# Kernel optimization log

Measured on AMD Instinct MI355X. Metric: run time of the kernel, lower is better.

The kernel has to match this reference:

```python
import jax, jax.numpy as jnp
import numpy as np

B, T, C = 4, 4096, 256

def setup_inputs() -> dict:
    key = jax.random.key(0)
    kx, km, kk, kq, kv = jax.random.split(key, 5)
    x = jax.random.normal(kx, (B, T, C), dtype=jnp.float32)
    mask = jax.random.randint(km, (B, T), 0, 2, dtype=jnp.int32)
    s = C ** -0.5
    Wk = jax.random.normal(kk, (C, C), dtype=jnp.float32) * s
    Wq = jax.random.normal(kq, (C, C), dtype=jnp.float32) * s
    Wv = jax.random.normal(kv, (C, C), dtype=jnp.float32) * s
    return {"x": x, "mask": mask, "Wk": Wk, "Wq": Wq, "Wv": Wv}

def reference(x, mask, Wk, Wq, Wv):
    # nn.Linear: y = x @ W.T  (W is [out, in])
    k = jnp.einsum('btc,dc->btd', x, Wk)   # [B,T,C]
    q = jnp.einsum('btc,dc->btd', x, Wq)   # [B,T,C]
    v = jnp.einsum('btc,dc->btd', x, Wv)   # [B,T,C]
    scale = k.shape[-1] ** -0.5
    weights = jnp.einsum('bqc,bkc->bqk', q, k) * scale  # [B,T,T]
    # torch quirk: mask.float().masked_fill(mask==0, -inf) adds +1.0 where mask!=0
    mask_f = jnp.where(mask == 0, -jnp.inf, mask.astype(weights.dtype))  # [B,T]
    masked = weights + mask_f[:, None, :]   # broadcast over query dim == repeat(1,T,1)
    attn = jax.nn.softmax(masked, axis=-1)
    out = jnp.einsum('bqk,bkc->bqc', attn, v)  # [B,T,C]
    return out
```

## Files before the change

### kernel.cpp

```cpp
#include <hip/hip_runtime.h>


typedef __attribute__((ext_vector_type(8)))  _Float16 f16x8;
typedef __attribute__((ext_vector_type(4)))  _Float16 f16x4;
typedef __attribute__((ext_vector_type(4)))  float    f32x4;
typedef __attribute__((ext_vector_type(16))) float    f32x16;

constexpr int Bb = 4;
constexpr int Tt = 4096;
constexpr int Cc = 256;
constexpr int BT = Bb * Tt;

#define MFMA16(a, b, c) __builtin_amdgcn_mfma_f32_16x16x32_f16((a), (b), (c), 0, 0, 0)
#define MFMA32(a, b, c) __builtin_amdgcn_mfma_f32_32x32x16_f16((a), (b), (c), 0, 0, 0)

__global__ __launch_bounds__(256) void qkv_proj(
    const float* __restrict__ x,
    const float* __restrict__ Wq, const float* __restrict__ Wk,
    const float* __restrict__ Wv,
    _Float16* __restrict__ qo, _Float16* __restrict__ ko,
    _Float16* __restrict__ vto)
{
    extern __shared__ _Float16 sm[];
    _Float16* xs = sm;
    _Float16* wsm = sm + 128 * 264;

    const int tid = threadIdx.x;
    const int m0  = blockIdx.x * 128;
    const int ny  = blockIdx.y;
    const int mat = ny >> 1;
    const int d0  = (ny & 1) * 128;
    const float* W = (mat == 0) ? Wq : (mat == 1 ? Wk : Wv);

#pragma unroll
    for (int i = 0; i < 32; ++i) {
        int flat = i * 256 + tid;
        int r = flat >> 6, c4 = (flat & 63) << 2;
        float4 v = *reinterpret_cast<const float4*>(x + (size_t)(m0 + r) * Cc + c4);
        f16x4 h = { (_Float16)v.x, (_Float16)v.y, (_Float16)v.z, (_Float16)v.w };
        *reinterpret_cast<f16x4*>(xs + r * 264 + c4) = h;
    }
#pragma unroll
    for (int i = 0; i < 32; ++i) {
        int flat = i * 256 + tid;
        int r = flat >> 6, c4 = (flat & 63) << 2;
        float4 v = *reinterpret_cast<const float4*>(W + (size_t)(d0 + r) * Cc + c4);
        f16x4 h = { (_Float16)v.x, (_Float16)v.y, (_Float16)v.z, (_Float16)v.w };
        *reinterpret_cast<f16x4*>(wsm + r * 264 + c4) = h;
    }
    __syncthreads();

    const int w = tid >> 6, lane = tid & 63;
    const int lr = lane & 15, lg = lane >> 4;

    f32x4 acc[2][8] = {};

#pragma unroll
    for (int kc = 0; kc < 8; ++kc) {
        const int c0 = kc * 32 + lg * 8;
        f16x8 xf[2], wf[8];
#pragma unroll
        for (int mb = 0; mb < 2; ++mb)
            xf[mb] = *reinterpret_cast<const f16x8*>(xs + (w * 32 + mb * 16 + lr) * 264 + c0);
#pragma unroll
        for (int db = 0; db < 8; ++db)
            wf[db] = *reinterpret_cast<const f16x8*>(wsm + (db * 16 + lr) * 264 + c0);
        if (mat != 2) {
#pragma unroll
            for (int mb = 0; mb < 2; ++mb)
#pragma unroll
                for (int db = 0; db < 8; ++db)
                    acc[mb][db] = MFMA16(wf[db], xf[mb], acc[mb][db]);
        } else {
#pragma unroll
            for (int mb = 0; mb < 2; ++mb)
#pragma unroll
                for (int db = 0; db < 8; ++db)
                    acc[mb][db] = MFMA16(xf[mb], wf[db], acc[mb][db]);
        }
    }

    if (mat != 2) {
        const float sc = (mat == 0) ? 0.0625f : 1.0f;
        const int jj  = (lg & 1) * 4;
#pragma unroll
        for (int mb = 0; mb < 2; ++mb)
#pragma unroll
            for (int db = 0; db < 8; ++db) {
                int m  = m0 + w * 32 + mb * 16 + lr;
                int c  = d0 + db * 16 + lg * 4;
                int kc = c >> 5;
                int ch = (c >> 3) & 3;
                f32x4 a = acc[mb][db];
                f16x4 h = { (_Float16)(a.x * sc), (_Float16)(a.y * sc),
                            (_Float16)(a.z * sc), (_Float16)(a.w * sc) };
                if (mat == 0) {
                    size_t off = (size_t)(m >> 5) * 8192 + (((m >> 4) & 1) * 8 + kc) * 512
                               + ch * 128 + (m & 15) * 8 + jj;
                    *reinterpret_cast<f16x4*>(qo + off) = h;
                } else {
                    size_t off = (size_t)(m >> 4) * 4096 + kc * 512
                               + ch * 128 + (m & 15) * 8 + jj;
                    *reinterpret_cast<f16x4*>(ko + off) = h;
                }
            }
    } else {
        const int jj = (lg & 1) * 4;
        const int kh = (lg >> 1) & 1;
#pragma unroll
        for (int mb = 0; mb < 2; ++mb)
#pragma unroll
            for (int db = 0; db < 8; ++db) {
                int d = d0 + db * 16 + lr;
                int m = m0 + w * 32 + mb * 16 + lg * 4;
                f32x4 a = acc[mb][db];
                f16x4 h = { (_Float16)a.x, (_Float16)a.y, (_Float16)a.z, (_Float16)a.w };
                size_t off = (size_t)(m >> 4) * 4096 + (d >> 5) * 512
                           + kh * 256 + (d & 31) * 8 + jj;
                *reinterpret_cast<f16x4*>(vto + off) = h;
            }
    }
}

__global__ __launch_bounds__(256, 1) void attn_kernel(
    const _Float16* __restrict__ qb, const _Float16* __restrict__ kb,
    const _Float16* __restrict__ vtb, const int* __restrict__ mask,
    float* __restrict__ outp)
{
    extern __shared__ char smraw[];
    float* mex  = (float*)(smraw + 6144);
    float* lex  = (float*)(smraw + 6656);
    float* oexf = (float*)(smraw + 8192);

    const int tid = threadIdx.x, w = tid >> 6, lane = tid & 63;
    const int qw = w >> 1, g = w & 1;
    const int l15 = lane & 15, l4 = lane >> 4;
    const int l31 = lane & 31, l5 = lane >> 5;

    const int bid = blockIdx.x;
    const int b   = (bid & 7) >> 1;
    const int qt  = ((bid >> 3) << 1) | (bid & 1);
    const int q0  = qt * 64;
    const size_t base = (size_t)b * Tt * Cc;
    const int* maskb = mask + (size_t)b * Tt;
    const _Float16* kTb = kb + base;
    const _Float16* vTb = vtb + base;

    f16x8 qf[2][8];
    {
        const _Float16* qTb = qb + (size_t)(b * 128 + qt * 2 + qw) * 8192;
#pragma unroll
        for (int qh = 0; qh < 2; ++qh)
#pragma unroll
            for (int kc = 0; kc < 8; ++kc)
                qf[qh][kc] = *reinterpret_cast<const f16x8*>(
                    qTb + (qh * 8 + kc) * 512 + l4 * 128 + l15 * 8);
    }

    _Float16* pw = (_Float16*)smraw + w * 768;

    f32x16 o[8] = {};
    float m0r = -60.f, m1r = -60.f, l0r = 0.f, l1r = 0.f;

    auto LOADT = [&](f16x8 (&kr)[8], f16x8 (&vr)[8], int4& mc, int tile) {
        const _Float16* kp = kTb + (size_t)tile * 4096 + l4 * 128 + l15 * 8;
#pragma unroll
        for (int kc = 0; kc < 8; ++kc)
            kr[kc] = *reinterpret_cast<const f16x8*>(kp + kc * 512);
        const _Float16* vp = vTb + (size_t)tile * 4096 + l5 * 256 + l31 * 8;
#pragma unroll
        for (int dt = 0; dt < 8; ++dt)
            vr[dt] = *reinterpret_cast<const f16x8*>(vp + dt * 512);
        mc = *reinterpret_cast<const int4*>(maskb + tile * 16 + l4 * 4);
    };

    auto COMPUTE = [&](f16x8 (&kr)[8], f16x8 (&vr)[8], int4 mc) {
        f32x4 s40 = { 0.f, 0.f, 0.f, 0.f }, s41 = { 0.f, 0.f, 0.f, 0.f };
#pragma unroll
        for (int kc = 0; kc < 8; ++kc) {
            s40 = MFMA16(kr[kc], qf[0][kc], s40);
            s41 = MFMA16(kr[kc], qf[1][kc], s41);
        }
        if (mc.x == 0) { s40[0] = -1e30f; s41[0] = -1e30f; }
        if (mc.y == 0) { s40[1] = -1e30f; s41[1] = -1e30f; }
        if (mc.z == 0) { s40[2] = -1e30f; s41[2] = -1e30f; }
        if (mc.w == 0) { s40[3] = -1e30f; s41[3] = -1e30f; }

        float t0 = fmaxf(fmaxf(s40[0], s40[1]), fmaxf(s40[2], s40[3]));
        float t1 = fmaxf(fmaxf(s41[0], s41[1]), fmaxf(s41[2], s41[3]));
        t0 = fmaxf(t0, __shfl_xor(t0, 16, 64)); t0 = fmaxf(t0, __shfl_xor(t0, 32, 64));
        t1 = fmaxf(t1, __shfl_xor(t1, 16, 64)); t1 = fmaxf(t1, __shfl_xor(t1, 32, 64));

        if (__any(t0 > m0r + 8.f || t1 > m1r + 8.f)) {
            float mn0 = fmaxf(m0r, t0), mn1 = fmaxf(m1r, t1);
            float c0 = __expf(m0r - mn0), c1 = __expf(m1r - mn1);
            m0r = mn0; m1r = mn1; l0r *= c0; l1r *= c1;
            float cs = (lane & 16) ? c1 : c0;
#pragma unroll
            for (int dt = 0; dt < 8; ++dt) o[dt] *= cs;
        }

        float rs0 = 0.f, rs1 = 0.f;
#pragma unroll
        for (int r = 0; r < 4; ++r) {
            float p0 = __expf(s40[r] - m0r); s40[r] = p0; rs0 += p0;
            float p1 = __expf(s41[r] - m1r); s41[r] = p1; rs1 += p1;
        }
        rs0 += __shfl_xor(rs0, 16, 64); rs0 += __shfl_xor(rs0, 32, 64);
        rs1 += __shfl_xor(rs1, 16, 64); rs1 += __shfl_xor(rs1, 32, 64);
        l0r += rs0; l1r += rs1;

        {
            f16x4 h0 = { (_Float16)s40[0], (_Float16)s40[1], (_Float16)s40[2], (_Float16)s40[3] };
            f16x4 h1 = { (_Float16)s41[0], (_Float16)s41[1], (_Float16)s41[2], (_Float16)s41[3] };
            *reinterpret_cast<f16x4*>(pw + l15 * 24 + l4 * 4)        = h0;
            *reinterpret_cast<f16x4*>(pw + (16 + l15) * 24 + l4 * 4) = h1;
        }
        f16x8 pf = *reinterpret_cast<const f16x8*>(pw + l31 * 24 + l5 * 8);

#pragma unroll
        for (int dt = 0; dt < 8; ++dt)
            o[dt] = MFMA32(vr[dt], pf, o[dt]);
    };

    f16x8 kA[8], vA[8], kB[8], vB[8];
    int4 mA_, mB_;
    const int ktb = g * 128;
    LOADT(kA, vA, mA_, ktb);
#pragma unroll 1
    for (int t2 = 0; t2 < 64; ++t2) {
        LOADT(kB, vB, mB_, ktb + 2 * t2 + 1);
        COMPUTE(kA, vA, mA_);
        LOADT(kA, vA, mA_, (2 * t2 + 2 < 128) ? (ktb + 2 * t2 + 2) : ktb);
        COMPUTE(kB, vB, mB_);
    }

    __syncthreads();
    if (l4 == 0) {
        mex[w * 32 + l15]      = m0r;  mex[w * 32 + 16 + l15] = m1r;
        lex[w * 32 + l15]      = l0r;  lex[w * 32 + 16 + l15] = l1r;
    }
    __syncthreads();

    {
        float mq  = (lane & 16) ? m1r : m0r;
        float mA2 = mex[(qw * 2 + 0) * 32 + l31];
        float mB2 = mex[(qw * 2 + 1) * 32 + l31];
        float mst = fmaxf(mA2, mB2);
        float osc = __expf(mq - mst);
        float* oq = oexf + qw * (32 * 258);
        if (g == 1) {
#pragma unroll
            for (int dt = 0; dt < 8; ++dt)
#pragma unroll
                for (int r = 0; r < 16; ++r) {
                    int d = dt * 32 + (r & 3) + 8 * (r >> 2) + 4 * l5;
                    oq[l31 * 258 + d] = o[dt][r] * osc;
                }
        }
        __syncthreads();
        if (g == 0) {
#pragma unroll
            for (int dt = 0; dt < 8; ++dt)
#pragma unroll
                for (int r = 0; r < 16; ++r) {
                    int d = dt * 32 + (r & 3) + 8 * (r >> 2) + 4 * l5;
                    oq[l31 * 258 + d] += o[dt][r] * osc;
                }
        }
        __syncthreads();
    }

    {
        const int q = tid >> 2, ds0 = (tid & 3) * 64;
        const int qws = q >> 5, ql = q & 31;
        float mA2 = mex[(qws * 2 + 0) * 32 + ql];
        float mB2 = mex[(qws * 2 + 1) * 32 + ql];
        float ms  = fmaxf(mA2, mB2);
        float lt  = lex[(qws * 2 + 0) * 32 + ql] * __expf(mA2 - ms)
                  + lex[(qws * 2 + 1) * 32 + ql] * __expf(mB2 - ms);
        float inv = 1.f / lt;
        const float* src = oexf + qws * (32 * 258) + ql * 258 + ds0;
        float* dst = outp + base + (size_t)(q0 + q) * Cc + ds0;
#pragma unroll
        for (int i = 0; i < 16; ++i) {
            f32x4 a = *reinterpret_cast<const f32x4*>(src + 4 * i);
            a[0] *= inv; a[1] *= inv; a[2] *= inv; a[3] *= inv;
            *reinterpret_cast<f32x4*>(dst + 4 * i) = a;
        }
    }
}

extern "C" void kernel_launch(void* const* d_in, const int* in_sizes, int n_in,
                              void* d_out, int out_size, void* d_ws, size_t ws_size,
                              hipStream_t stream)
{
    (void)in_sizes; (void)n_in; (void)out_size; (void)ws_size;
    const float* x   = (const float*)d_in[0];
    const int*  mask = (const int*)d_in[1];
    const float* Wk  = (const float*)d_in[2];
    const float* Wq  = (const float*)d_in[3];
    const float* Wv  = (const float*)d_in[4];
    float* out = (float*)d_out;

    _Float16* q  = (_Float16*)d_ws;
    _Float16* k  = q + (size_t)BT * Cc;
    _Float16* vt = k + (size_t)BT * Cc;

    dim3 gA(128, 6), blkA(256);
    size_t ldsA = (size_t)(128 + 128) * 264 * sizeof(_Float16);
    qkv_proj<<<gA, blkA, ldsA, stream>>>(x, Wq, Wk, Wv, q, k, vt);

    dim3 gB(256), blkB(256);
    size_t ldsB = 74240;
    attn_kernel<<<gB, blkB, ldsB, stream>>>(q, k, vt, mask, out);
}
```

Before: 128.5 us.

## Split attention work across head-dim halves, double blocks, use exp2 softmax

The attention kernel now handles 32 queries per block instead of 64. Each pair of waves splits the 256-wide value dimension into two halves, which halves the output accumulators and value registers. The launch goes to 512 blocks with launch bounds of 2 and a smaller LDS footprint. Value loads move inside the compute step rather than being double-buffered. The Q scale now folds in log2(e) so softmax can use exp2f, the rescale threshold is loosened to match, and the row-sum shuffle reduction is deferred until after the loop. These changes aim for higher occupancy and less per-iteration shuffle work. The costs are duplicated QK^T computation across the two d-halves and less latency hiding for the V loads.

```diff
diff --git a/kernel.cpp b/kernel.cpp
--- a/kernel.cpp
+++ b/kernel.cpp
@@ -81,7 +81,7 @@
     }
 
     if (mat != 2) {
-        const float sc = (mat == 0) ? 0.0625f : 1.0f;
+        const float sc = (mat == 0) ? 0.0625f * 1.44269504f : 1.0f;
         const int jj  = (lg & 1) * 4;
 #pragma unroll
         for (int mb = 0; mb < 2; ++mb)
@@ -122,25 +122,25 @@
     }
 }
 
-__global__ __launch_bounds__(256, 1) void attn_kernel(
+__global__ __launch_bounds__(256, 2) void attn_kernel(
     const _Float16* __restrict__ qb, const _Float16* __restrict__ kb,
     const _Float16* __restrict__ vtb, const int* __restrict__ mask,
     float* __restrict__ outp)
 {
     extern __shared__ char smraw[];
     float* mex  = (float*)(smraw + 6144);
-    float* lex  = (float*)(smraw + 6656);
-    float* oexf = (float*)(smraw + 8192);
+    float* lex  = (float*)(smraw + 6400);
+    float* oexf = (float*)(smraw + 6656);
 
     const int tid = threadIdx.x, w = tid >> 6, lane = tid & 63;
-    const int qw = w >> 1, g = w & 1;
+    const int dh = w & 1, g = w >> 1;
     const int l15 = lane & 15, l4 = lane >> 4;
     const int l31 = lane & 31, l5 = lane >> 5;
 
     const int bid = blockIdx.x;
     const int b   = (bid & 7) >> 1;
     const int qt  = ((bid >> 3) << 1) | (bid & 1);
-    const int q0  = qt * 64;
+    const int q0  = qt * 32;
     const size_t base = (size_t)b * Tt * Cc;
     const int* maskb = mask + (size_t)b * Tt;
     const _Float16* kTb = kb + base;
@@ -148,7 +148,7 @@
 
     f16x8 qf[2][8];
     {
-        const _Float16* qTb = qb + (size_t)(b * 128 + qt * 2 + qw) * 8192;
+        const _Float16* qTb = qb + (size_t)(b * 128 + qt) * 8192;
 #pragma unroll
         for (int qh = 0; qh < 2; ++qh)
 #pragma unroll
@@ -159,22 +159,27 @@
 
     _Float16* pw = (_Float16*)smraw + w * 768;
 
-    f32x16 o[8] = {};
+    f32x16 o[4] = {};
     float m0r = -60.f, m1r = -60.f, l0r = 0.f, l1r = 0.f;
 
-    auto LOADT = [&](f16x8 (&kr)[8], f16x8 (&vr)[8], int4& mc, int tile) {
+    auto LOADK = [&](f16x8 (&kr)[8], int4& mc, int tile) {
         const _Float16* kp = kTb + (size_t)tile * 4096 + l4 * 128 + l15 * 8;
 #pragma unroll
         for (int kc = 0; kc < 8; ++kc)
             kr[kc] = *reinterpret_cast<const f16x8*>(kp + kc * 512);
-        const _Float16* vp = vTb + (size_t)tile * 4096 + l5 * 256 + l31 * 8;
-#pragma unroll
-        for (int dt = 0; dt < 8; ++dt)
-            vr[dt] = *reinterpret_cast<const f16x8*>(vp + dt * 512);
         mc = *reinterpret_cast<const int4*>(maskb + tile * 16 + l4 * 4);
     };
 
-    auto COMPUTE = [&](f16x8 (&kr)[8], f16x8 (&vr)[8], int4 mc) {
+    f16x8 vr[4];
+    auto COMPUTE = [&](f16x8 (&kr)[8], int4 mc, int tile) {
+        {
+            const _Float16* vp = vTb + (size_t)tile * 4096 + dh * 2048
+                               + l5 * 256 + l31 * 8;
+#pragma unroll
+            for (int dt = 0; dt < 4; ++dt)
+                vr[dt] = *reinterpret_cast<const f16x8*>(vp + dt * 512);
+        }
+
         f32x4 s40 = { 0.f, 0.f, 0.f, 0.f }, s41 = { 0.f, 0.f, 0.f, 0.f };
 #pragma unroll
         for (int kc = 0; kc < 8; ++kc) {
@@ -186,29 +191,25 @@
         if (mc.z == 0) { s40[2] = -1e30f; s41[2] = -1e30f; }
         if (mc.w == 0) { s40[3] = -1e30f; s41[3] = -1e30f; }
 
-        float t0 = fmaxf(fmaxf(s40[0], s40[1]), fmaxf(s40[2], s40[3]));
-        float t1 = fmaxf(fmaxf(s41[0], s41[1]), fmaxf(s41[2], s41[3]));
-        t0 = fmaxf(t0, __shfl_xor(t0, 16, 64)); t0 = fmaxf(t0, __shfl_xor(t0, 32, 64));
-        t1 = fmaxf(t1, __shfl_xor(t1, 16, 64)); t1 = fmaxf(t1, __shfl_xor(t1, 32, 64));
-
-        if (__any(t0 > m0r + 8.f || t1 > m1r + 8.f)) {
+        float t0l = fmaxf(fmaxf(s40[0], s40[1]), fmaxf(s40[2], s40[3]));
+        float t1l = fmaxf(fmaxf(s41[0], s41[1]), fmaxf(s41[2], s41[3]));
+        if (__any(t0l > m0r + 11.54f || t1l > m1r + 11.54f)) {
+            float t0 = t0l, t1 = t1l;
+            t0 = fmaxf(t0, __shfl_xor(t0, 16, 64)); t0 = fmaxf(t0, __shfl_xor(t0, 32, 64));
+            t1 = fmaxf(t1, __shfl_xor(t1, 16, 64)); t1 = fmaxf(t1, __shfl_xor(t1, 32, 64));
             float mn0 = fmaxf(m0r, t0), mn1 = fmaxf(m1r, t1);
-            float c0 = __expf(m0r - mn0), c1 = __expf(m1r - mn1);
+            float c0 = exp2f(m0r - mn0), c1 = exp2f(m1r - mn1);
             m0r = mn0; m1r = mn1; l0r *= c0; l1r *= c1;
             float cs = (lane & 16) ? c1 : c0;
 #pragma unroll
-            for (int dt = 0; dt < 8; ++dt) o[dt] *= cs;
-        }
-
-        float rs0 = 0.f, rs1 = 0.f;
+            for (int dt = 0; dt < 4; ++dt) o[dt] *= cs;
+        }
+
 #pragma unroll
         for (int r = 0; r < 4; ++r) {
-            float p0 = __expf(s40[r] - m0r); s40[r] = p0; rs0 += p0;
-            float p1 = __expf(s41[r] - m1r); s41[r] = p1; rs1 += p1;
-        }
-        rs0 += __shfl_xor(rs0, 16, 64); rs0 += __shfl_xor(rs0, 32, 64);
-        rs1 += __shfl_xor(rs1, 16, 64); rs1 += __shfl_xor(rs1, 32, 64);
-        l0r += rs0; l1r += rs1;
+            float p0 = exp2f(s40[r] - m0r); s40[r] = p0; l0r += p0;
+            float p1 = exp2f(s41[r] - m1r); s41[r] = p1; l1r += p1;
+        }
 
         {
             f16x4 h0 = { (_Float16)s40[0], (_Float16)s40[1], (_Float16)s40[2], (_Float16)s40[3] };
@@ -219,71 +220,69 @@
         f16x8 pf = *reinterpret_cast<const f16x8*>(pw + l31 * 24 + l5 * 8);
 
 #pragma unroll
-        for (int dt = 0; dt < 8; ++dt)
+        for (int dt = 0; dt < 4; ++dt)
             o[dt] = MFMA32(vr[dt], pf, o[dt]);
     };
 
-    f16x8 kA[8], vA[8], kB[8], vB[8];
+    f16x8 kA[8], kB[8];
     int4 mA_, mB_;
     const int ktb = g * 128;
-    LOADT(kA, vA, mA_, ktb);
+    LOADK(kA, mA_, ktb);
 #pragma unroll 1
     for (int t2 = 0; t2 < 64; ++t2) {
-        LOADT(kB, vB, mB_, ktb + 2 * t2 + 1);
-        COMPUTE(kA, vA, mA_);
-        LOADT(kA, vA, mA_, (2 * t2 + 2 < 128) ? (ktb + 2 * t2 + 2) : ktb);
-        COMPUTE(kB, vB, mB_);
-    }
-
+        LOADK(kB, mB_, ktb + 2 * t2 + 1);
+        COMPUTE(kA, mA_, ktb + 2 * t2);
+        LOADK(kA, mA_, (2 * t2 + 2 < 128) ? (ktb + 2 * t2 + 2) : ktb);
+        COMPUTE(kB, mB_, ktb + 2 * t2 + 1);
+    }
+
+    float L0 = l0r; L0 += __shfl_xor(L0, 16, 64); L0 += __shfl_xor(L0, 32, 64);
+    float L1 = l1r; L1 += __shfl_xor(L1, 16, 64); L1 += __shfl_xor(L1, 32, 64);
+
+    if (dh == 0 && l4 == 0) {
+        mex[g * 32 + l15]      = m0r;  mex[g * 32 + 16 + l15] = m1r;
+        lex[g * 32 + l15]      = L0;   lex[g * 32 + 16 + l15] = L1;
+    }
     __syncthreads();
-    if (l4 == 0) {
-        mex[w * 32 + l15]      = m0r;  mex[w * 32 + 16 + l15] = m1r;
-        lex[w * 32 + l15]      = l0r;  lex[w * 32 + 16 + l15] = l1r;
-    }
-    __syncthreads();
 
     {
+        float mst = fmaxf(mex[l31], mex[32 + l31]);
         float mq  = (lane & 16) ? m1r : m0r;
-        float mA2 = mex[(qw * 2 + 0) * 32 + l31];
-        float mB2 = mex[(qw * 2 + 1) * 32 + l31];
-        float mst = fmaxf(mA2, mB2);
-        float osc = __expf(mq - mst);
-        float* oq = oexf + qw * (32 * 258);
+        float osc = exp2f(mq - mst);
+        float* oq = oexf + dh * 4224;
         if (g == 1) {
 #pragma unroll
-            for (int dt = 0; dt < 8; ++dt)
+            for (int dt = 0; dt < 4; ++dt)
 #pragma unroll
                 for (int r = 0; r < 16; ++r) {
-                    int d = dt * 32 + (r & 3) + 8 * (r >> 2) + 4 * l5;
-                    oq[l31 * 258 + d] = o[dt][r] * osc;
+                    int dloc = dt * 32 + (r & 3) + 8 * (r >> 2) + 4 * l5;
+                    oq[l31 * 132 + dloc] = o[dt][r] * osc;
                 }
         }
         __syncthreads();
         if (g == 0) {
 #pragma unroll
-            for (int dt = 0; dt < 8; ++dt)
+            for (int dt = 0; dt < 4; ++dt)
 #pragma unroll
                 for (int r = 0; r < 16; ++r) {
-                    int d = dt * 32 + (r & 3) + 8 * (r >> 2) + 4 * l5;
-                    oq[l31 * 258 + d] += o[dt][r] * osc;
+                    int dloc = dt * 32 + (r & 3) + 8 * (r >> 2) + 4 * l5;
+                    oq[l31 * 132 + dloc] += o[dt][r] * osc;
                 }
         }
         __syncthreads();
     }
 
     {
-        const int q = tid >> 2, ds0 = (tid & 3) * 64;
-        const int qws = q >> 5, ql = q & 31;
-        float mA2 = mex[(qws * 2 + 0) * 32 + ql];
-        float mB2 = mex[(qws * 2 + 1) * 32 + ql];
+        const int q = tid >> 3, seg = tid & 7;
+        const int ds0 = seg * 32, dhr = seg >> 2, dl0 = (seg & 3) * 32;
+        float mA2 = mex[q], mB2 = mex[32 + q];
         float ms  = fmaxf(mA2, mB2);
-        float lt  = lex[(qws * 2 + 0) * 32 + ql] * __expf(mA2 - ms)
-                  + lex[(qws * 2 + 1) * 32 + ql] * __expf(mB2 - ms);
+        float lt  = lex[q] * exp2f(mA2 - ms) + lex[32 + q] * exp2f(mB2 - ms);
         float inv = 1.f / lt;
-        const float* src = oexf + qws * (32 * 258) + ql * 258 + ds0;
+        const float* src = oexf + dhr * 4224 + q * 132 + dl0;
         float* dst = outp + base + (size_t)(q0 + q) * Cc + ds0;
 #pragma unroll
-        for (int i = 0; i < 16; ++i) {
+        for (int i = 0; i < 8; ++i) {
             f32x4 a = *reinterpret_cast<const f32x4*>(src + 4 * i);
             a[0] *= inv; a[1] *= inv; a[2] *= inv; a[3] *= inv;
             *reinterpret_cast<f32x4*>(dst + 4 * i) = a;
@@ -311,7 +310,7 @@
     size_t ldsA = (size_t)(128 + 128) * 264 * sizeof(_Float16);
     qkv_proj<<<gA, blkA, ldsA, stream>>>(x, Wq, Wk, Wv, q, k, vt);
 
-    dim3 gB(256), blkB(256);
-    size_t ldsB = 74240;
+    dim3 gB(512), blkB(256);
+    size_t ldsB = 40448;
     attn_kernel<<<gB, blkB, ldsB, stream>>>(q, k, vt, mask, out);
 }
```

Result: slower. 157.2 us (+22.4%).

## Feed P to PV MFMA from registers using 16x16x16 and exp2 softmax

Applied to the files above, without the earlier changes.

Reworks the PV product to use 16x16x16 MFMAs whose A operand is the score accumulator layout directly, which removes the LDS round trip for the probability tile. The V layout from the projection kernel changes to match, and the query scale folds in log2(e) so the softmax can use exp2. Row sums are kept per lane and reduced only once at the end. The max reduction across lanes now runs only when a rescale is triggered. The QK accumulation is split into two chains to increase MFMA ILP. In exchange it issues twice as many smaller MFMAs for PV and adds shuffles to broadcast the rescale factors.

```diff
diff --git a/kernel.cpp b/kernel.cpp
--- a/kernel.cpp
+++ b/kernel.cpp
@@ -4,15 +4,14 @@
 typedef __attribute__((ext_vector_type(8)))  _Float16 f16x8;
 typedef __attribute__((ext_vector_type(4)))  _Float16 f16x4;
 typedef __attribute__((ext_vector_type(4)))  float    f32x4;
-typedef __attribute__((ext_vector_type(16))) float    f32x16;
 
 constexpr int Bb = 4;
 constexpr int Tt = 4096;
 constexpr int Cc = 256;
 constexpr int BT = Bb * Tt;
 
-#define MFMA16(a, b, c) __builtin_amdgcn_mfma_f32_16x16x32_f16((a), (b), (c), 0, 0, 0)
-#define MFMA32(a, b, c) __builtin_amdgcn_mfma_f32_32x32x16_f16((a), (b), (c), 0, 0, 0)
+#define MFMA16(a, b, c)   __builtin_amdgcn_mfma_f32_16x16x32_f16((a), (b), (c), 0, 0, 0)
+#define MFMA1616(a, b, c) __builtin_amdgcn_mfma_f32_16x16x16f16((a), (b), (c), 0, 0, 0)
 
 __global__ __launch_bounds__(256) void qkv_proj(
     const float* __restrict__ x,
@@ -81,7 +80,7 @@
     }
 
     if (mat != 2) {
-        const float sc = (mat == 0) ? 0.0625f : 1.0f;
+        const float sc = (mat == 0) ? 0.0625f * 1.44269504f : 1.0f;
         const int jj  = (lg & 1) * 4;
 #pragma unroll
         for (int mb = 0; mb < 2; ++mb)
@@ -105,8 +104,6 @@
                 }
             }
     } else {
-        const int jj = (lg & 1) * 4;
-        const int kh = (lg >> 1) & 1;
 #pragma unroll
         for (int mb = 0; mb < 2; ++mb)
 #pragma unroll
@@ -115,8 +112,8 @@
                 int m = m0 + w * 32 + mb * 16 + lg * 4;
                 f32x4 a = acc[mb][db];
                 f16x4 h = { (_Float16)a.x, (_Float16)a.y, (_Float16)a.z, (_Float16)a.w };
-                size_t off = (size_t)(m >> 4) * 4096 + (d >> 5) * 512
-                           + kh * 256 + (d & 31) * 8 + jj;
+                size_t off = (size_t)(m >> 4) * 4096 + (size_t)(d >> 4) * 256
+                           + lg * 64 + (d & 15) * 4;
                 *reinterpret_cast<f16x4*>(vto + off) = h;
             }
     }
@@ -128,14 +125,13 @@
     float* __restrict__ outp)
 {
     extern __shared__ char smraw[];
-    float* mex  = (float*)(smraw + 6144);
-    float* lex  = (float*)(smraw + 6656);
-    float* oexf = (float*)(smraw + 8192);
+    float* mex  = (float*)(smraw);
+    float* lex  = (float*)(smraw + 512);
+    float* oexf = (float*)(smraw + 1024);
 
     const int tid = threadIdx.x, w = tid >> 6, lane = tid & 63;
     const int qw = w >> 1, g = w & 1;
     const int l15 = lane & 15, l4 = lane >> 4;
-    const int l31 = lane & 31, l5 = lane >> 5;
 
     const int bid = blockIdx.x;
     const int b   = (bid & 7) >> 1;
@@ -157,73 +153,78 @@
                     qTb + (qh * 8 + kc) * 512 + l4 * 128 + l15 * 8);
     }
 
-    _Float16* pw = (_Float16*)smraw + w * 768;
-
-    f32x16 o[8] = {};
+    f32x4 o[2][16] = {};
     float m0r = -60.f, m1r = -60.f, l0r = 0.f, l1r = 0.f;
 
-    auto LOADT = [&](f16x8 (&kr)[8], f16x8 (&vr)[8], int4& mc, int tile) {
+    auto LOADT = [&](f16x8 (&kr)[8], f16x4 (&vr)[16], int4& mc, int tile) {
         const _Float16* kp = kTb + (size_t)tile * 4096 + l4 * 128 + l15 * 8;
 #pragma unroll
         for (int kc = 0; kc < 8; ++kc)
             kr[kc] = *reinterpret_cast<const f16x8*>(kp + kc * 512);
-        const _Float16* vp = vTb + (size_t)tile * 4096 + l5 * 256 + l31 * 8;
-#pragma unroll
-        for (int dt = 0; dt < 8; ++dt)
-            vr[dt] = *reinterpret_cast<const f16x8*>(vp + dt * 512);
+        const _Float16* vp = vTb + (size_t)tile * 4096 + l4 * 64 + l15 * 4;
+#pragma unroll
+        for (int dt = 0; dt < 16; ++dt)
+            vr[dt] = *reinterpret_cast<const f16x4*>(vp + dt * 256);
         mc = *reinterpret_cast<const int4*>(maskb + tile * 16 + l4 * 4);
     };
 
-    auto COMPUTE = [&](f16x8 (&kr)[8], f16x8 (&vr)[8], int4 mc) {
-        f32x4 s40 = { 0.f, 0.f, 0.f, 0.f }, s41 = { 0.f, 0.f, 0.f, 0.f };
-#pragma unroll
-        for (int kc = 0; kc < 8; ++kc) {
-            s40 = MFMA16(kr[kc], qf[0][kc], s40);
-            s41 = MFMA16(kr[kc], qf[1][kc], s41);
-        }
+    auto COMPUTE = [&](f16x8 (&kr)[8], f16x4 (&vr)[16], int4 mc) {
+        f32x4 a0 = { 0.f, 0.f, 0.f, 0.f }, b0 = { 0.f, 0.f, 0.f, 0.f };
+        f32x4 a1 = { 0.f, 0.f, 0.f, 0.f }, b1 = { 0.f, 0.f, 0.f, 0.f };
+#pragma unroll
+        for (int kc = 0; kc < 4; ++kc) {
+            a0 = MFMA16(kr[kc], qf[0][kc], a0);
+            a1 = MFMA16(kr[kc], qf[1][kc], a1);
+        }
+#pragma unroll
+        for (int kc = 4; kc < 8; ++kc) {
+            b0 = MFMA16(kr[kc], qf[0][kc], b0);
+            b1 = MFMA16(kr[kc], qf[1][kc], b1);
+        }
+        f32x4 s40 = a0 + b0, s41 = a1 + b1;
+
         if (mc.x == 0) { s40[0] = -1e30f; s41[0] = -1e30f; }
         if (mc.y == 0) { s40[1] = -1e30f; s41[1] = -1e30f; }
         if (mc.z == 0) { s40[2] = -1e30f; s41[2] = -1e30f; }
         if (mc.w == 0) { s40[3] = -1e30f; s41[3] = -1e30f; }
 
-        float t0 = fmaxf(fmaxf(s40[0], s40[1]), fmaxf(s40[2], s40[3]));
-        float t1 = fmaxf(fmaxf(s41[0], s41[1]), fmaxf(s41[2], s41[3]));
-        t0 = fmaxf(t0, __shfl_xor(t0, 16, 64)); t0 = fmaxf(t0, __shfl_xor(t0, 32, 64));
-        t1 = fmaxf(t1, __shfl_xor(t1, 16, 64)); t1 = fmaxf(t1, __shfl_xor(t1, 32, 64));
-
-        if (__any(t0 > m0r + 8.f || t1 > m1r + 8.f)) {
+        float t0l = fmaxf(fmaxf(s40[0], s40[1]), fmaxf(s40[2], s40[3]));
+        float t1l = fmaxf(fmaxf(s41[0], s41[1]), fmaxf(s41[2], s41[3]));
+        if (__any(t0l > m0r + 11.54f || t1l > m1r + 11.54f)) {
+            float t0 = t0l, t1 = t1l;
+            t0 = fmaxf(t0, __shfl_xor(t0, 16, 64)); t0 = fmaxf(t0, __shfl_xor(t0, 32, 64));
+            t1 = fmaxf(t1, __shfl_xor(t1, 16, 64)); t1 = fmaxf(t1, __shfl_xor(t1, 32, 64));
             float mn0 = fmaxf(m0r, t0), mn1 = fmaxf(m1r, t1);
-            float c0 = __expf(m0r - mn0), c1 = __expf(m1r - mn1);
+            float c0 = exp2f(m0r - mn0), c1 = exp2f(m1r - mn1);
             m0r = mn0; m1r = mn1; l0r *= c0; l1r *= c1;
-            float cs = (lane & 16) ? c1 : c0;
-#pragma unroll
-            for (int dt = 0; dt < 8; ++dt) o[dt] *= cs;
-        }
-
-        float rs0 = 0.f, rs1 = 0.f;
+            f32x4 cv0, cv1;
+#pragma unroll
+            for (int r = 0; r < 4; ++r) {
+                cv0[r] = __shfl(c0, l4 * 4 + r, 64);
+                cv1[r] = __shfl(c1, l4 * 4 + r, 64);
+            }
+#pragma unroll
+            for (int dt = 0; dt < 16; ++dt) { o[0][dt] *= cv0; o[1][dt] *= cv1; }
+        }
+
 #pragma unroll
         for (int r = 0; r < 4; ++r) {
-            float p0 = __expf(s40[r] - m0r); s40[r] = p0; rs0 += p0;
-            float p1 = __expf(s41[r] - m1r); s41[r] = p1; rs1 += p1;
-        }
-        rs0 += __shfl_xor(rs0, 16, 64); rs0 += __shfl_xor(rs0, 32, 64);
-        rs1 += __shfl_xor(rs1, 16, 64); rs1 += __shfl_xor(rs1, 32, 64);
-        l0r += rs0; l1r += rs1;
-
-        {
-            f16x4 h0 = { (_Float16)s40[0], (_Float16)s40[1], (_Float16)s40[2], (_Float16)s40[3] };
-            f16x4 h1 = { (_Float16)s41[0], (_Float16)s41[1], (_Float16)s41[2], (_Float16)s41[3] };
-            *reinterpret_cast<f16x4*>(pw + l15 * 24 + l4 * 4)        = h0;
-            *reinterpret_cast<f16x4*>(pw + (16 + l15) * 24 + l4 * 4) = h1;
-        }
-        f16x8 pf = *reinterpret_cast<const f16x8*>(pw + l31 * 24 + l5 * 8);
-
-#pragma unroll
-        for (int dt = 0; dt < 8; ++dt)
-            o[dt] = MFMA32(vr[dt], pf, o[dt]);
+            float p0 = exp2f(s40[r] - m0r); s40[r] = p0; l0r += p0;
+            float p1 = exp2f(s41[r] - m1r); s41[r] = p1; l1r += p1;
+        }
+
+        f16x4 pa0 = { (_Float16)s40[0], (_Float16)s40[1], (_Float16)s40[2], (_Float16)s40[3] };
+        f16x4 pa1 = { (_Float16)s41[0], (_Float16)s41[1], (_Float16)s41[2], (_Float16)s41[3] };
+
+#pragma unroll
+        for (int dt = 0; dt < 16; ++dt) {
+            o[0][dt] = MFMA1616(pa0, vr[dt], o[0][dt]);
+            o[1][dt] = MFMA1616(pa1, vr[dt], o[1][dt]);
+        }
     };
 
-    f16x8 kA[8], vA[8], kB[8], vB[8];
+    f16x8 kA[8], kB[8];
+    f16x4 vA[16], vB[16];
     int4 mA_, mB_;
     const int ktb = g * 128;
     LOADT(kA, vA, mA_, ktb);
@@ -235,38 +236,48 @@
         COMPUTE(kB, vB, mB_);
     }
 
+    float L0 = l0r; L0 += __shfl_xor(L0, 16, 64); L0 += __shfl_xor(L0, 32, 64);
+    float L1 = l1r; L1 += __shfl_xor(L1, 16, 64); L1 += __shfl_xor(L1, 32, 64);
+
     __syncthreads();
-    if (l4 == 0) {
-        mex[w * 32 + l15]      = m0r;  mex[w * 32 + 16 + l15] = m1r;
-        lex[w * 32 + l15]      = l0r;  lex[w * 32 + 16 + l15] = l1r;
+    if (lane < 16) {
+        mex[w * 32 + lane]      = m0r;  mex[w * 32 + 16 + lane] = m1r;
+        lex[w * 32 + lane]      = L0;   lex[w * 32 + 16 + lane] = L1;
     }
     __syncthreads();
 
     {
-        float mq  = (lane & 16) ? m1r : m0r;
-        float mA2 = mex[(qw * 2 + 0) * 32 + l31];
-        float mB2 = mex[(qw * 2 + 1) * 32 + l31];
-        float mst = fmaxf(mA2, mB2);
-        float osc = __expf(mq - mst);
         float* oq = oexf + qw * (32 * 258);
+        f32x4 osc[2];
+#pragma unroll
+        for (int qh = 0; qh < 2; ++qh)
+#pragma unroll
+            for (int r = 0; r < 4; ++r) {
+                int qq = qh * 16 + l4 * 4 + r;
+                float mO = mex[(qw * 2 + g) * 32 + qq];
+                float mX = mex[(qw * 2 + (1 - g)) * 32 + qq];
+                osc[qh][r] = exp2f(mO - fmaxf(mO, mX));
+            }
         if (g == 1) {
 #pragma unroll
-            for (int dt = 0; dt < 8; ++dt)
-#pragma unroll
-                for (int r = 0; r < 16; ++r) {
-                    int d = dt * 32 + (r & 3) + 8 * (r >> 2) + 4 * l5;
-                    oq[l31 * 258 + d] = o[dt][r] * osc;
-                }
+            for (int qh = 0; qh < 2; ++qh)
+#pragma unroll
+                for (int dt = 0; dt < 16; ++dt)
+#pragma unroll
+                    for (int r = 0; r < 4; ++r)
+                        oq[(qh * 16 + l4 * 4 + r) * 258 + dt * 16 + l15]
+                            = o[qh][dt][r] * osc[qh][r];
         }
         __syncthreads();
         if (g == 0) {
 #pragma unroll
-            for (int dt = 0; dt < 8; ++dt)
-#pragma unroll
-                for (int r = 0; r < 16; ++r) {
-                    int d = dt * 32 + (r & 3) + 8 * (r >> 2) + 4 * l5;
-                    oq[l31 * 258 + d] += o[dt][r] * osc;
-                }
+            for (int qh = 0; qh < 2; ++qh)
+#pragma unroll
+                for (int dt = 0; dt < 16; ++dt)
+#pragma unroll
+                    for (int r = 0; r < 4; ++r)
+                        oq[(qh * 16 + l4 * 4 + r) * 258 + dt * 16 + l15]
+                            += o[qh][dt][r] * osc[qh][r];
         }
         __syncthreads();
     }
@@ -277,8 +288,8 @@
         float mA2 = mex[(qws * 2 + 0) * 32 + ql];
         float mB2 = mex[(qws * 2 + 1) * 32 + ql];
         float ms  = fmaxf(mA2, mB2);
-        float lt  = lex[(qws * 2 + 0) * 32 + ql] * __expf(mA2 - ms)
-                  + lex[(qws * 2 + 1) * 32 + ql] * __expf(mB2 - ms);
+        float lt  = lex[(qws * 2 + 0) * 32 + ql] * exp2f(mA2 - ms)
+                  + lex[(qws * 2 + 1) * 32 + ql] * exp2f(mB2 - ms);
         float inv = 1.f / lt;
         const float* src = oexf + qws * (32 * 258) + ql * 258 + ds0;
         float* dst = outp + base + (size_t)(q0 + q) * Cc + ds0;
@@ -312,6 +323,6 @@
     qkv_proj<<<gA, blkA, ldsA, stream>>>(x, Wq, Wk, Wv, q, k, vt);
 
     dim3 gB(256), blkB(256);
-    size_t ldsB = 74240;
+    size_t ldsB = 67072;
     attn_kernel<<<gB, blkB, ldsB, stream>>>(q, k, vt, mask, out);
 }
```

Result: slower. 141.7 us (+10.3%).
